# Kernel optimization log

Hardware: AMD Instinct MI355X
Metric: run time of the kernel (lower is better)

## Reference

```python
import jax, jax.numpy as jnp
import numpy as np

B, T, U, D = 2, 512, 48, 512
H, K = 1024, 128  # hidden_channels, num_classes; fc1 in = 2*D = 1024


def setup_inputs() -> dict:
    key = jax.random.key(0)
    ks = jax.random.split(key, 9)
    s = 0.02
    return {
        "img_feature": jax.random.normal(ks[0], (B, T, D), jnp.float32),
        "label_feature": jax.random.normal(ks[1], (B, U, D), jnp.float32),
        "masks": jnp.ones((B, 1, T), jnp.float32),
        "W1": jax.random.normal(ks[2], (H, 2 * D), jnp.float32) * s,
        "b1": jnp.zeros((H,), jnp.float32),
        "W2": jax.random.normal(ks[3], (K, H), jnp.float32) * s,
        "b2": jnp.zeros((K,), jnp.float32),
        "conv_w": jax.random.normal(ks[4], (K, D), jnp.float32) * s,
        "conv_b": jnp.zeros((K,), jnp.float32),
    }


def reference(img_feature, label_feature, masks, W1, b1, W2, b2, conv_w, conv_b):
    # pointwise Conv1d over img features: (B,T,D) -> (B,K,T), masked
    img_seg_score = (jnp.einsum('btd,kd->bkt', img_feature, conv_w)
                     + conv_b[None, :, None]) * masks
    # fc1(cat(label, img)) == label @ Wl^T + img @ Wi^T + b1 (broadcast add),
    # avoiding the O(B*U*T*2D) repeat+cat intermediate.
    d = label_feature.shape[-1]
    Wl, Wi = W1[:, :d], W1[:, d:]
    lab = jnp.einsum('bud,hd->buh', label_feature, Wl)  # (B,U,H)
    img = jnp.einsum('btd,hd->bth', img_feature, Wi)    # (B,T,H)
    h = jnp.tanh(lab[:, :, None, :] + img[:, None, :, :] + b1)  # (B,U,T,H)
    joint = jnp.einsum('buth,kh->butk', h, W2) + b2
    joint_score = jax.nn.log_softmax(joint, axis=-1)
    return (img_seg_score, joint_score)
```

## Files before the change

kernel.cpp:

```cpp
#include <hip/hip_runtime.h>
#include <math.h>

#define BB 2
#define TT 512
#define UU 48
#define DD 512
#define HH 1024
#define KK 128

typedef _Float16 f16x8 __attribute__((ext_vector_type(8)));
typedef __fp16 fp16x2_t __attribute__((ext_vector_type(2)));
typedef float floatx4 __attribute__((ext_vector_type(4)));

__device__ __forceinline__ f16x8 tanh8z(f16x8 z) {
    f16x8 o;
#pragma unroll
    for (int i = 0; i < 8; i += 2) {
        float e0 = __builtin_amdgcn_exp2f((float)z[i]);
        float e1 = __builtin_amdgcn_exp2f((float)z[i + 1]);
        float r0 = __builtin_amdgcn_rcpf(e0 + 1.0f);
        float r1 = __builtin_amdgcn_rcpf(e1 + 1.0f);
        fp16x2_t p = __builtin_amdgcn_cvt_pkrtz(fmaf(-2.0f, r0, 1.0f),
                                                fmaf(-2.0f, r1, 1.0f));
        o[i] = (_Float16)p[0];
        o[i + 1] = (_Float16)p[1];
    }
    return o;
}

__global__ __launch_bounds__(256) void mid_kernel5(
    const float* __restrict__ img, const float* __restrict__ labf,
    const float* __restrict__ W1, const float* __restrict__ W2,
    const float* __restrict__ conv_w,
    const float* __restrict__ b1, const float* __restrict__ conv_b,
    const float* __restrict__ masks,
    _Float16* __restrict__ imgHf, _Float16* __restrict__ labHf,
    _Float16* __restrict__ W2s, float* __restrict__ seg_out) {
    int bid = blockIdx.x, tid = threadIdx.x;
    if (bid >= 624) {
        int base = (bid - 624) * 256 + tid;
#pragma unroll
        for (int i = 0; i < 32; ++i) {
            int o = base + i * 4096;
            int hg = o >> 10, kk2 = (o >> 3) & 127, hl = o & 7;
            W2s[o] = (_Float16)W2[(size_t)kk2 * HH + hg * 8 + hl];
        }
        return;
    }
    __shared__ __align__(16) _Float16 a_s[32][72];
    __shared__ __align__(16) _Float16 w_s[4096];
    const float* Arow;
    const float* Wbase;
    int r0, n0b, wstride, region;
    if (bid < 512) {
        region = 0; Arow = img; Wbase = W1 + 512; wstride = 2 * DD;
        int xcd = bid & 7, j = bid >> 3;
        r0 = (j & 31) * 32; n0b = (xcd * 2 + (j >> 5)) * 64;
    } else if (bid < 560) {
        region = 1; Arow = labf; Wbase = W1; wstride = 2 * DD;
        int i = bid - 512; r0 = (i % 3) * 32; n0b = (i / 3) * 64;
    } else {
        region = 2; Arow = img; Wbase = conv_w; wstride = DD;
        int i = bid - 560; r0 = (i >> 1) * 32; n0b = (i & 1) * 64;
    }
    int lane = tid & 63, wv = tid >> 6;
    int m0 = (wv & 1) * 16, n0w = (wv >> 1) * 32;
    int q = lane >> 4, r = lane & 15;
    int arow = tid >> 3, acol = (tid & 7) * 8;
    int wn = tid >> 2, wk0 = (tid & 3) * 16;
    const float* aptr = &Arow[(size_t)(r0 + arow) * DD + acol];
    const float* wptr = &Wbase[(size_t)(n0b + wn) * wstride + wk0];
    floatx4 acc[2] = {};
    float4 pa0, pa1, pw[4];
    pa0 = *(const float4*)aptr;
    pa1 = *(const float4*)(aptr + 4);
#pragma unroll
    for (int i2 = 0; i2 < 4; ++i2) pw[i2] = *(const float4*)(wptr + i2 * 4);
    for (int c = 0; c < 8; ++c) {
        f16x8 av;
        av[0] = (_Float16)pa0.x; av[1] = (_Float16)pa0.y;
        av[2] = (_Float16)pa0.z; av[3] = (_Float16)pa0.w;
        av[4] = (_Float16)pa1.x; av[5] = (_Float16)pa1.y;
        av[6] = (_Float16)pa1.z; av[7] = (_Float16)pa1.w;
        *(f16x8*)&a_s[arow][acol] = av;
        f16x8 w0, w1;
        w0[0] = (_Float16)pw[0].x; w0[1] = (_Float16)pw[0].y;
        w0[2] = (_Float16)pw[0].z; w0[3] = (_Float16)pw[0].w;
        w0[4] = (_Float16)pw[1].x; w0[5] = (_Float16)pw[1].y;
        w0[6] = (_Float16)pw[1].z; w0[7] = (_Float16)pw[1].w;
        w1[0] = (_Float16)pw[2].x; w1[1] = (_Float16)pw[2].y;
        w1[2] = (_Float16)pw[2].z; w1[3] = (_Float16)pw[2].w;
        w1[4] = (_Float16)pw[3].x; w1[5] = (_Float16)pw[3].y;
        w1[6] = (_Float16)pw[3].z; w1[7] = (_Float16)pw[3].w;
        int kg = wk0 >> 3;
        *(f16x8*)&w_s[((kg + 0) * 64 + wn) * 8] = w0;
        *(f16x8*)&w_s[((kg + 1) * 64 + wn) * 8] = w1;
        __syncthreads();
        if (c < 7) {
            int cb = (c + 1) * 64;
            pa0 = *(const float4*)(aptr + cb);
            pa1 = *(const float4*)(aptr + cb + 4);
#pragma unroll
            for (int i2 = 0; i2 < 4; ++i2)
                pw[i2] = *(const float4*)(wptr + cb + i2 * 4);
        }
#pragma unroll
        for (int kt = 0; kt < 2; ++kt) {
            f16x8 af = *(const f16x8*)&a_s[m0 + r][kt * 32 + q * 8];
#pragma unroll
            for (int nt = 0; nt < 2; ++nt) {
                f16x8 bf = *(const f16x8*)
                    &w_s[((kt * 4 + q) * 64 + n0w + nt * 16 + r) * 8];
                acc[nt] = __builtin_amdgcn_mfma_f32_16x16x32_f16(
                    af, bf, acc[nt], 0, 0, 0);
            }
        }
        __syncthreads();
    }
    const float SC = 2.8853900817779268f;
    if (region == 0) {
#pragma unroll
        for (int nt = 0; nt < 2; ++nt) {
            int n = n0b + n0w + nt * 16 + r;
#pragma unroll
            for (int rr = 0; rr < 4; ++rr)
                imgHf[(size_t)(r0 + m0 + 4 * q + rr) * HH + n] =
                    (_Float16)(acc[nt][rr] * SC);
        }
    } else if (region == 1) {
#pragma unroll
        for (int nt = 0; nt < 2; ++nt) {
            int n = n0b + n0w + nt * 16 + r;
            float bv = b1[n];
#pragma unroll
            for (int rr = 0; rr < 4; ++rr)
                labHf[(size_t)(r0 + m0 + 4 * q + rr) * HH + n] =
                    (_Float16)((acc[nt][rr] + bv) * SC);
        }
    } else {
#pragma unroll
        for (int nt = 0; nt < 2; ++nt) {
            int k = n0b + n0w + nt * 16 + r;
            float bv = conv_b[k];
#pragma unroll
            for (int rr = 0; rr < 4; ++rr) {
                int row = r0 + m0 + 4 * q + rr;
                int b = row >> 9, t = row & 511;
                seg_out[((size_t)b * KK + k) * TT + t] =
                    (acc[nt][rr] + bv) * masks[row];
            }
        }
    }
}

__global__ __launch_bounds__(384, 2) void joint_kernel9(
    const _Float16* __restrict__ imgHf,
    const _Float16* __restrict__ labHf,
    const _Float16* __restrict__ W2s,
    const float* __restrict__ b2,
    float* __restrict__ out) {
    __shared__ __align__(16) _Float16 w_s[2][32768];
    int tid = threadIdx.x, bid = blockIdx.x;
    int lane = tid & 63, wv = tid >> 6;
    int ql = lane >> 4, r = lane & 15;
    int g0 = bid * 192 + wv * 32;
    int gr0 = g0 + r, gr1 = g0 + 16 + r;
    int bu0 = gr0 >> 9, t0 = gr0 & 511;
    int bu1 = gr1 >> 9, t1 = gr1 & 511;
    const _Float16* ir0 = imgHf + (size_t)(((bu0 >= UU) ? TT : 0) + t0) * HH;
    const _Float16* ir1 = imgHf + (size_t)(((bu1 >= UU) ? TT : 0) + t1) * HH;
    const _Float16* lr0 = labHf + (size_t)bu0 * HH;
    const _Float16* lr1 = labHf + (size_t)bu1 * HH;
    int c0 = ql * 8, c1 = 32 + ql * 8;
    floatx4 acc0[8] = {}, acc1[8] = {};
#pragma unroll
    for (int k2 = 0; k2 < 10; ++k2)
        *(f16x8*)&w_s[0][(tid + k2 * 384) * 8] =
            *(const f16x8*)&W2s[(tid + k2 * 384) * 8];
    if (tid < 256)
        *(f16x8*)&w_s[0][(tid + 3840) * 8] =
            *(const f16x8*)&W2s[(tid + 3840) * 8];
    f16x8 i0A = *(const f16x8*)&ir0[c0], i0B = *(const f16x8*)&ir0[c1];
    f16x8 i1A = *(const f16x8*)&ir1[c0], i1B = *(const f16x8*)&ir1[c1];
    f16x8 l0A = *(const f16x8*)&lr0[c0], l0B = *(const f16x8*)&lr0[c1];
    f16x8 l1A = *(const f16x8*)&lr1[c0], l1B = *(const f16x8*)&lr1[c1];
    __syncthreads();
    int buf = 0;
    for (int qq = 0; qq < 4; ++qq) {
        f16x8 wr[11];
        if (qq < 3) {
            const _Float16* wsrc = W2s + (size_t)(qq + 1) * 32768;
#pragma unroll
            for (int k2 = 0; k2 < 10; ++k2)
                wr[k2] = *(const f16x8*)&wsrc[(tid + k2 * 384) * 8];
            if (tid < 256) wr[10] = *(const f16x8*)&wsrc[(tid + 3840) * 8];
        }
        const _Float16* wb = w_s[buf];
#pragma unroll
        for (int c = 0; c < 4; ++c) {
            int cc = qq * 4 + c;
            f16x8 ni0A, ni0B, ni1A, ni1B, nl0A, nl0B, nl1A, nl1B;
            if (cc < 15) {
                int cb = (cc + 1) * 64;
                ni0A = *(const f16x8*)&ir0[cb + c0];
                ni0B = *(const f16x8*)&ir0[cb + c1];
                ni1A = *(const f16x8*)&ir1[cb + c0];
                ni1B = *(const f16x8*)&ir1[cb + c1];
                nl0A = *(const f16x8*)&lr0[cb + c0];
                nl0B = *(const f16x8*)&lr0[cb + c1];
                nl1A = *(const f16x8*)&lr1[cb + c0];
                nl1B = *(const f16x8*)&lr1[cb + c1];
            }
            f16x8 a0A = tanh8z(i0A + l0A);
            f16x8 a1A = tanh8z(i1A + l1A);
#pragma unroll
            for (int nt = 0; nt < 8; ++nt) {
                f16x8 bf = *(const f16x8*)
                    &wb[c * 8192 + (ql * 128 + nt * 16 + r) * 8];
                acc0[nt] = __builtin_amdgcn_mfma_f32_16x16x32_f16(
                    a0A, bf, acc0[nt], 0, 0, 0);
                acc1[nt] = __builtin_amdgcn_mfma_f32_16x16x32_f16(
                    a1A, bf, acc1[nt], 0, 0, 0);
            }
            f16x8 a0B = tanh8z(i0B + l0B);
            f16x8 a1B = tanh8z(i1B + l1B);
#pragma unroll
            for (int nt = 0; nt < 8; ++nt) {
                f16x8 bf = *(const f16x8*)
                    &wb[c * 8192 + ((4 + ql) * 128 + nt * 16 + r) * 8];
                acc0[nt] = __builtin_amdgcn_mfma_f32_16x16x32_f16(
                    a0B, bf, acc0[nt], 0, 0, 0);
                acc1[nt] = __builtin_amdgcn_mfma_f32_16x16x32_f16(
                    a1B, bf, acc1[nt], 0, 0, 0);
            }
            if (cc < 15) {
                i0A = ni0A; i0B = ni0B; i1A = ni1A; i1B = ni1B;
                l0A = nl0A; l0B = nl0B; l1A = nl1A; l1B = nl1B;
            }
        }
        if (qq < 3) {
            _Float16* wd = w_s[buf ^ 1];
#pragma unroll
            for (int k2 = 0; k2 < 10; ++k2)
                *(f16x8*)&wd[(tid + k2 * 384) * 8] = wr[k2];
            if (tid < 256) *(f16x8*)&wd[(tid + 3840) * 8] = wr[10];
            __syncthreads();
            buf ^= 1;
        }
    }
    float b2v[8];
#pragma unroll
    for (int nt = 0; nt < 8; ++nt) b2v[nt] = b2[nt * 16 + r];
#pragma unroll
    for (int mt = 0; mt < 2; ++mt) {
        float* obase = out + (size_t)(g0 + mt * 16 + 4 * ql) * KK;
#pragma unroll
        for (int rr = 0; rr < 4; ++rr) {
            float v[8];
            float mx = -INFINITY;
#pragma unroll
            for (int nt = 0; nt < 8; ++nt) {
                v[nt] = (mt ? acc1[nt][rr] : acc0[nt][rr]) + b2v[nt];
                mx = fmaxf(mx, v[nt]);
            }
            mx = fmaxf(mx, __shfl_xor(mx, 1, 16));
            mx = fmaxf(mx, __shfl_xor(mx, 2, 16));
            mx = fmaxf(mx, __shfl_xor(mx, 4, 16));
            mx = fmaxf(mx, __shfl_xor(mx, 8, 16));
            float s = 0.f;
#pragma unroll
            for (int nt = 0; nt < 8; ++nt) s += __expf(v[nt] - mx);
            s += __shfl_xor(s, 1, 16);
            s += __shfl_xor(s, 2, 16);
            s += __shfl_xor(s, 4, 16);
            s += __shfl_xor(s, 8, 16);
            float lse = mx + __logf(s);
#pragma unroll
            for (int nt = 0; nt < 8; ++nt)
                obase[(size_t)rr * KK + nt * 16 + r] = v[nt] - lse;
        }
    }
}

extern "C" void kernel_launch(void* const* d_in, const int* in_sizes, int n_in,
                              void* d_out, int out_size, void* d_ws, size_t ws_size,
                              hipStream_t stream) {
    const float* img    = (const float*)d_in[0];
    const float* labf   = (const float*)d_in[1];
    const float* masks  = (const float*)d_in[2];
    const float* W1     = (const float*)d_in[3];
    const float* b1     = (const float*)d_in[4];
    const float* W2     = (const float*)d_in[5];
    const float* b2     = (const float*)d_in[6];
    const float* conv_w = (const float*)d_in[7];
    const float* conv_b = (const float*)d_in[8];
    float* out = (float*)d_out;

    _Float16* base  = (_Float16*)d_ws;
    _Float16* imgHf = base;
    _Float16* labHf = imgHf + 1024 * 1024;
    _Float16* W2s   = labHf + 96 * 1024;

    mid_kernel5<<<640, 256, 0, stream>>>(img, labf, W1, W2, conv_w,
                                         b1, conv_b, masks,
                                         imgHf, labHf, W2s, out);
    joint_kernel9<<<256, 384, 0, stream>>>(imgHf, labHf, W2s, b2,
                                           out + (size_t)BB * KK * TT);
}
```

Baseline: 124.5 us.

## Load full K-extent of projection GEMM tiles into LDS in one shot

```diff
diff --git a/kernel.cpp b/kernel.cpp
--- a/kernel.cpp
+++ b/kernel.cpp
@@ -28,7 +28,7 @@
     return o;
 }
 
-__global__ __launch_bounds__(256) void mid_kernel5(
+__global__ __launch_bounds__(256) void mid_kernel6(
     const float* __restrict__ img, const float* __restrict__ labf,
     const float* __restrict__ W1, const float* __restrict__ W2,
     const float* __restrict__ conv_w,
@@ -47,8 +47,8 @@
         }
         return;
     }
-    __shared__ __align__(16) _Float16 a_s[32][72];
-    __shared__ __align__(16) _Float16 w_s[4096];
+    __shared__ __align__(16) _Float16 a_s[32][520];
+    __shared__ __align__(16) _Float16 w_s[32768];
     const float* Arow;
     const float* Wbase;
     int r0, n0b, wstride, region;
@@ -66,56 +66,54 @@
     int lane = tid & 63, wv = tid >> 6;
     int m0 = (wv & 1) * 16, n0w = (wv >> 1) * 32;
     int q = lane >> 4, r = lane & 15;
-    int arow = tid >> 3, acol = (tid & 7) * 8;
+    int arow = tid >> 3, acol = (tid & 7) * 64;
     int wn = tid >> 2, wk0 = (tid & 3) * 16;
-    const float* aptr = &Arow[(size_t)(r0 + arow) * DD + acol];
-    const float* wptr = &Wbase[(size_t)(n0b + wn) * wstride + wk0];
-    floatx4 acc[2] = {};
-    float4 pa0, pa1, pw[4];
-    pa0 = *(const float4*)aptr;
-    pa1 = *(const float4*)(aptr + 4);
-#pragma unroll
-    for (int i2 = 0; i2 < 4; ++i2) pw[i2] = *(const float4*)(wptr + i2 * 4);
+    const float* ap = &Arow[(size_t)(r0 + arow) * DD + acol];
+    const float* wp = &Wbase[(size_t)(n0b + wn) * wstride + wk0];
+    float4 pa[16], pw[32];
+#pragma unroll
+    for (int j = 0; j < 16; ++j) pa[j] = *(const float4*)(ap + j * 4);
+#pragma unroll
+    for (int c = 0; c < 8; ++c)
+#pragma unroll
+        for (int j = 0; j < 4; ++j)
+            pw[c * 4 + j] = *(const float4*)(wp + c * 64 + j * 4);
+#pragma unroll
+    for (int j = 0; j < 8; ++j) {
+        f16x8 v;
+        v[0] = (_Float16)pa[2 * j].x; v[1] = (_Float16)pa[2 * j].y;
+        v[2] = (_Float16)pa[2 * j].z; v[3] = (_Float16)pa[2 * j].w;
+        v[4] = (_Float16)pa[2 * j + 1].x; v[5] = (_Float16)pa[2 * j + 1].y;
+        v[6] = (_Float16)pa[2 * j + 1].z; v[7] = (_Float16)pa[2 * j + 1].w;
+        *(f16x8*)&a_s[arow][acol + j * 8] = v;
+    }
+#pragma unroll
     for (int c = 0; c < 8; ++c) {
-        f16x8 av;
-        av[0] = (_Float16)pa0.x; av[1] = (_Float16)pa0.y;
-        av[2] = (_Float16)pa0.z; av[3] = (_Float16)pa0.w;
-        av[4] = (_Float16)pa1.x; av[5] = (_Float16)pa1.y;
-        av[6] = (_Float16)pa1.z; av[7] = (_Float16)pa1.w;
-        *(f16x8*)&a_s[arow][acol] = av;
+        int kg = c * 8 + (tid & 3) * 2;
         f16x8 w0, w1;
-        w0[0] = (_Float16)pw[0].x; w0[1] = (_Float16)pw[0].y;
-        w0[2] = (_Float16)pw[0].z; w0[3] = (_Float16)pw[0].w;
-        w0[4] = (_Float16)pw[1].x; w0[5] = (_Float16)pw[1].y;
-        w0[6] = (_Float16)pw[1].z; w0[7] = (_Float16)pw[1].w;
-        w1[0] = (_Float16)pw[2].x; w1[1] = (_Float16)pw[2].y;
-        w1[2] = (_Float16)pw[2].z; w1[3] = (_Float16)pw[2].w;
-        w1[4] = (_Float16)pw[3].x; w1[5] = (_Float16)pw[3].y;
-        w1[6] = (_Float16)pw[3].z; w1[7] = (_Float16)pw[3].w;
-        int kg = wk0 >> 3;
+        w0[0] = (_Float16)pw[c * 4 + 0].x; w0[1] = (_Float16)pw[c * 4 + 0].y;
+        w0[2] = (_Float16)pw[c * 4 + 0].z; w0[3] = (_Float16)pw[c * 4 + 0].w;
+        w0[4] = (_Float16)pw[c * 4 + 1].x; w0[5] = (_Float16)pw[c * 4 + 1].y;
+        w0[6] = (_Float16)pw[c * 4 + 1].z; w0[7] = (_Float16)pw[c * 4 + 1].w;
+        w1[0] = (_Float16)pw[c * 4 + 2].x; w1[1] = (_Float16)pw[c * 4 + 2].y;
+        w1[2] = (_Float16)pw[c * 4 + 2].z; w1[3] = (_Float16)pw[c * 4 + 2].w;
+        w1[4] = (_Float16)pw[c * 4 + 3].x; w1[5] = (_Float16)pw[c * 4 + 3].y;
+        w1[6] = (_Float16)pw[c * 4 + 3].z; w1[7] = (_Float16)pw[c * 4 + 3].w;
         *(f16x8*)&w_s[((kg + 0) * 64 + wn) * 8] = w0;
         *(f16x8*)&w_s[((kg + 1) * 64 + wn) * 8] = w1;
-        __syncthreads();
-        if (c < 7) {
-            int cb = (c + 1) * 64;
-            pa0 = *(const float4*)(aptr + cb);
-            pa1 = *(const float4*)(aptr + cb + 4);
-#pragma unroll
-            for (int i2 = 0; i2 < 4; ++i2)
-                pw[i2] = *(const float4*)(wptr + cb + i2 * 4);
-        }
-#pragma unroll
-        for (int kt = 0; kt < 2; ++kt) {
-            f16x8 af = *(const f16x8*)&a_s[m0 + r][kt * 32 + q * 8];
-#pragma unroll
-            for (int nt = 0; nt < 2; ++nt) {
-                f16x8 bf = *(const f16x8*)
-                    &w_s[((kt * 4 + q) * 64 + n0w + nt * 16 + r) * 8];
-                acc[nt] = __builtin_amdgcn_mfma_f32_16x16x32_f16(
-                    af, bf, acc[nt], 0, 0, 0);
-            }
-        }
-        __syncthreads();
+    }
+    __syncthreads();
+    floatx4 acc[2] = {};
+#pragma unroll
+    for (int k = 0; k < 16; ++k) {
+        f16x8 af = *(const f16x8*)&a_s[m0 + r][k * 32 + q * 8];
+#pragma unroll
+        for (int nt = 0; nt < 2; ++nt) {
+            f16x8 bf = *(const f16x8*)
+                &w_s[((k * 4 + q) * 64 + n0w + nt * 16 + r) * 8];
+            acc[nt] = __builtin_amdgcn_mfma_f32_16x16x32_f16(
+                af, bf, acc[nt], 0, 0, 0);
+        }
     }
     const float SC = 2.8853900817779268f;
     if (region == 0) {
@@ -301,7 +299,7 @@
     _Float16* labHf = imgHf + 1024 * 1024;
     _Float16* W2s   = labHf + 96 * 1024;
 
-    mid_kernel5<<<640, 256, 0, stream>>>(img, labf, W1, W2, conv_w,
+    mid_kernel6<<<640, 256, 0, stream>>>(img, labf, W1, W2, conv_w,
                                          b1, conv_b, masks,
                                          imgHf, labHf, W2s, out);
     joint_kernel9<<<256, 384, 0, stream>>>(imgHf, labHf, W2s, b2,
```

After: 133.2 us. +7.0%, slower.

## Stream W2 tiles into LDS with direct global-to-LDS loads and batch activation prefetch

Applied to the files above, without the earlier changes.

```diff
diff --git a/kernel.cpp b/kernel.cpp
--- a/kernel.cpp
+++ b/kernel.cpp
@@ -11,6 +11,9 @@
 typedef _Float16 f16x8 __attribute__((ext_vector_type(8)));
 typedef __fp16 fp16x2_t __attribute__((ext_vector_type(2)));
 typedef float floatx4 __attribute__((ext_vector_type(4)));
+typedef __attribute__((address_space(3))) _Float16 lds_f16;
+typedef __attribute__((address_space(1))) const void g_cvoid;
+typedef __attribute__((address_space(3))) void l_void;
 
 __device__ __forceinline__ f16x8 tanh8z(f16x8 z) {
     f16x8 o;
@@ -153,7 +156,7 @@
     }
 }
 
-__global__ __launch_bounds__(384, 2) void joint_kernel9(
+__global__ __launch_bounds__(384, 2) void joint_kernel10(
     const _Float16* __restrict__ imgHf,
     const _Float16* __restrict__ labHf,
     const _Float16* __restrict__ W2s,
@@ -173,46 +176,48 @@
     const _Float16* lr1 = labHf + (size_t)bu1 * HH;
     int c0 = ql * 8, c1 = 32 + ql * 8;
     floatx4 acc0[8] = {}, acc1[8] = {};
-#pragma unroll
-    for (int k2 = 0; k2 < 10; ++k2)
-        *(f16x8*)&w_s[0][(tid + k2 * 384) * 8] =
-            *(const f16x8*)&W2s[(tid + k2 * 384) * 8];
-    if (tid < 256)
-        *(f16x8*)&w_s[0][(tid + 3840) * 8] =
-            *(const f16x8*)&W2s[(tid + 3840) * 8];
-    f16x8 i0A = *(const f16x8*)&ir0[c0], i0B = *(const f16x8*)&ir0[c1];
-    f16x8 i1A = *(const f16x8*)&ir1[c0], i1B = *(const f16x8*)&ir1[c1];
-    f16x8 l0A = *(const f16x8*)&lr0[c0], l0B = *(const f16x8*)&lr0[c1];
-    f16x8 l1A = *(const f16x8*)&lr1[c0], l1B = *(const f16x8*)&lr1[c1];
-    __syncthreads();
-    int buf = 0;
-    for (int qq = 0; qq < 4; ++qq) {
-        f16x8 wr[11];
-        if (qq < 3) {
-            const _Float16* wsrc = W2s + (size_t)(qq + 1) * 32768;
-#pragma unroll
-            for (int k2 = 0; k2 < 10; ++k2)
-                wr[k2] = *(const f16x8*)&wsrc[(tid + k2 * 384) * 8];
-            if (tid < 256) wr[10] = *(const f16x8*)&wsrc[(tid + 3840) * 8];
-        }
-        const _Float16* wb = w_s[buf];
+    f16x8 Ai[4][2][2], Al[4][2][2];
+
+    if (wv < 4) {
+        const _Float16* gs = W2s + (size_t)wv * 16 * 512 + lane * 8;
+        lds_f16* ls = (lds_f16*)&w_s[0][(size_t)wv * 16 * 512];
+#pragma unroll
+        for (int i = 0; i < 16; ++i)
+            __builtin_amdgcn_global_load_lds((g_cvoid*)(gs + i * 512),
+                                             (l_void*)(ls + i * 512), 16, 0, 0);
+    }
+#pragma unroll
+    for (int c = 0; c < 4; ++c) {
+        int cb = c * 64;
+        Ai[c][0][0] = *(const f16x8*)&ir0[cb + c0];
+        Ai[c][0][1] = *(const f16x8*)&ir0[cb + c1];
+        Ai[c][1][0] = *(const f16x8*)&ir1[cb + c0];
+        Ai[c][1][1] = *(const f16x8*)&ir1[cb + c1];
+        Al[c][0][0] = *(const f16x8*)&lr0[cb + c0];
+        Al[c][0][1] = *(const f16x8*)&lr0[cb + c1];
+        Al[c][1][0] = *(const f16x8*)&lr1[cb + c0];
+        Al[c][1][1] = *(const f16x8*)&lr1[cb + c1];
+    }
+    asm volatile("s_waitcnt vmcnt(0)" ::: "memory");
+    __builtin_amdgcn_s_barrier();
+    asm volatile("" ::: "memory");
+
+#pragma unroll
+    for (int qn = 0; qn < 4; ++qn) {
+        const _Float16* wb = w_s[qn & 1];
+        if (qn < 3 && wv < 4) {
+            const _Float16* gs = W2s + (size_t)(qn + 1) * 32768 +
+                                 (size_t)wv * 16 * 512 + lane * 8;
+            lds_f16* ls = (lds_f16*)&w_s[(qn + 1) & 1][(size_t)wv * 16 * 512];
+#pragma unroll
+            for (int i = 0; i < 16; ++i)
+                __builtin_amdgcn_global_load_lds(
+                    (g_cvoid*)(gs + i * 512), (l_void*)(ls + i * 512), 16, 0, 0);
+        }
 #pragma unroll
         for (int c = 0; c < 4; ++c) {
-            int cc = qq * 4 + c;
-            f16x8 ni0A, ni0B, ni1A, ni1B, nl0A, nl0B, nl1A, nl1B;
-            if (cc < 15) {
-                int cb = (cc + 1) * 64;
-                ni0A = *(const f16x8*)&ir0[cb + c0];
-                ni0B = *(const f16x8*)&ir0[cb + c1];
-                ni1A = *(const f16x8*)&ir1[cb + c0];
-                ni1B = *(const f16x8*)&ir1[cb + c1];
-                nl0A = *(const f16x8*)&lr0[cb + c0];
-                nl0B = *(const f16x8*)&lr0[cb + c1];
-                nl1A = *(const f16x8*)&lr1[cb + c0];
-                nl1B = *(const f16x8*)&lr1[cb + c1];
-            }
-            f16x8 a0A = tanh8z(i0A + l0A);
-            f16x8 a1A = tanh8z(i1A + l1A);
+            f16x8 a0A = tanh8z(Ai[c][0][0] + Al[c][0][0]);
+            f16x8 a1A = tanh8z(Ai[c][1][0] + Al[c][1][0]);
 #pragma unroll
             for (int nt = 0; nt < 8; ++nt) {
                 f16x8 bf = *(const f16x8*)
@@ -222,8 +227,8 @@
                 acc1[nt] = __builtin_amdgcn_mfma_f32_16x16x32_f16(
                     a1A, bf, acc1[nt], 0, 0, 0);
             }
-            f16x8 a0B = tanh8z(i0B + l0B);
-            f16x8 a1B = tanh8z(i1B + l1B);
+            f16x8 a0B = tanh8z(Ai[c][0][1] + Al[c][0][1]);
+            f16x8 a1B = tanh8z(Ai[c][1][1] + Al[c][1][1]);
 #pragma unroll
             for (int nt = 0; nt < 8; ++nt) {
                 f16x8 bf = *(const f16x8*)
@@ -233,19 +238,23 @@
                 acc1[nt] = __builtin_amdgcn_mfma_f32_16x16x32_f16(
                     a1B, bf, acc1[nt], 0, 0, 0);
             }
-            if (cc < 15) {
-                i0A = ni0A; i0B = ni0B; i1A = ni1A; i1B = ni1B;
-                l0A = nl0A; l0B = nl0B; l1A = nl1A; l1B = nl1B;
-            }
-        }
-        if (qq < 3) {
-            _Float16* wd = w_s[buf ^ 1];
-#pragma unroll
-            for (int k2 = 0; k2 < 10; ++k2)
-                *(f16x8*)&wd[(tid + k2 * 384) * 8] = wr[k2];
-            if (tid < 256) *(f16x8*)&wd[(tid + 3840) * 8] = wr[10];
-            __syncthreads();
-            buf ^= 1;
+        }
+        if (qn < 3) {
+#pragma unroll
+            for (int c = 0; c < 4; ++c) {
+                int cb = (qn + 1) * 256 + c * 64;
+                Ai[c][0][0] = *(const f16x8*)&ir0[cb + c0];
+                Ai[c][0][1] = *(const f16x8*)&ir0[cb + c1];
+                Ai[c][1][0] = *(const f16x8*)&ir1[cb + c0];
+                Ai[c][1][1] = *(const f16x8*)&ir1[cb + c1];
+                Al[c][0][0] = *(const f16x8*)&lr0[cb + c0];
+                Al[c][0][1] = *(const f16x8*)&lr0[cb + c1];
+                Al[c][1][0] = *(const f16x8*)&lr1[cb + c0];
+                Al[c][1][1] = *(const f16x8*)&lr1[cb + c1];
+            }
+            if (wv < 4) asm volatile("s_waitcnt vmcnt(32)" ::: "memory");
+            __builtin_amdgcn_s_barrier();
+            asm volatile("" ::: "memory");
         }
     }
     float b2v[8];
@@ -304,6 +313,6 @@
     mid_kernel5<<<640, 256, 0, stream>>>(img, labf, W1, W2, conv_w,
                                          b1, conv_b, masks,
                                          imgHf, labHf, W2s, out);
-    joint_kernel9<<<256, 384, 0, stream>>>(imgHf, labHf, W2s, b2,
-                                           out + (size_t)BB * KK * TT);
+    joint_kernel10<<<256, 384, 0, stream>>>(imgHf, labHf, W2s, b2,
+                                            out + (size_t)BB * KK * TT);
 }
```

Measured after the change: 123.7 us. About the same (-0.7%).
